# Performance work log

Measured on AMD Instinct MI355X. Metric: run time of the kernel, lower is better.

Reference implementation:

```python
import jax, jax.numpy as jnp
import numpy as np


def conv1x1(x, w, b):
    # x: [B,C,H,W], w: [O,C], b: [O] -> [B,O,H,W]
    return jnp.einsum('bchw,oc->bohw', x, w) + b[None, :, None, None]


def setup_inputs() -> dict:
    key = jax.random.key(0)
    ks = jax.random.split(key, 8)
    B, C, H, W = 16, 256, 64, 64
    Cq = C // 8
    x = jax.random.normal(ks[0], (B, C, H, W), dtype=jnp.float32)
    wq = jax.random.normal(ks[1], (Cq, C), dtype=jnp.float32) * (2.0 / C) ** 0.5
    bq = jnp.zeros((Cq,), dtype=jnp.float32)
    wk = jax.random.normal(ks[2], (Cq, C), dtype=jnp.float32) * (2.0 / C) ** 0.5
    bk = jnp.zeros((Cq,), dtype=jnp.float32)
    wv = jax.random.normal(ks[3], (C, C), dtype=jnp.float32) * (2.0 / C) ** 0.5
    bv = jnp.zeros((C,), dtype=jnp.float32)
    gamma = jax.random.normal(ks[4], (1,), dtype=jnp.float32) * 0.1
    return {'x': x, 'wq': wq, 'bq': bq, 'wk': wk, 'bk': bk, 'wv': wv, 'bv': bv, 'gamma': gamma}


def reference(x, wq, bq, wk, bk, wv, bv, gamma):
    B, C, H, W = x.shape
    bH = B // 4
    bW = B // 4  # requires bH*bW == B, i.e. B == 16
    q = conv1x1(x, wq, bq)   # [B, C/8, H, W]
    k = conv1x1(x, wk, bk)   # [B, C/8, H, W]
    v = conv1x1(x, wv, bv)   # [B, C, H, W]
    # batch index b -> grid (h = b // bW, w = b % bW); token feature = flat map
    qg = q.reshape(bH, bW, -1)  # [bH, bW, Dq]
    kg = k.reshape(bH, bW, -1)
    vg = v.reshape(bH, bW, -1)  # [bH, bW, Dv]
    # column ('H') attention with -inf diagonal, row ('W') attention
    eH = jnp.einsum('hwd,gwd->hwg', qg, kg)  # [bH, bW, bH]
    eye = jnp.eye(bH, dtype=bool)[:, None, :]  # mask h == h'
    eH = jnp.where(eye, -jnp.inf, eH)
    eW = jnp.einsum('hwd,hgd->hwg', qg, kg)  # [bH, bW, bW]
    att = jax.nn.softmax(jnp.concatenate([eH, eW], axis=-1), axis=-1)
    aH, aW = att[..., :bH], att[..., bH:]
    oH = jnp.einsum('hwg,gwd->hwd', aH, vg)  # attend down the column
    oW = jnp.einsum('hwg,hgd->hwd', aW, vg)  # attend along the row
    out = (oH + oW).reshape(B, C, H, W)
    return gamma[0] * out + x
```

## Files before the change

kernel.cpp:

```cpp
#include <hip/hip_runtime.h>

#define B_   16
#define C_   256
#define HW_  4096
#define DQK  131072
#define DV   1048576

using bf16x8  = __attribute__((ext_vector_type(8))) __bf16;
using ushort8 = __attribute__((ext_vector_type(8))) unsigned short;
using u16x4   = __attribute__((ext_vector_type(4))) unsigned short;
using f32x4   = __attribute__((ext_vector_type(4))) float;

static __device__ __forceinline__ unsigned short f2bf(float f) {
    union { float f; unsigned u; } v; v.f = f;
    unsigned r = v.u + 0x7FFFu + ((v.u >> 16) & 1u);
    return (unsigned short)(r >> 16);
}
static __device__ __forceinline__ float bf2f(unsigned short h) {
    union { unsigned u; float f; } v; v.u = ((unsigned)h) << 16;
    return v.f;
}

__global__ __launch_bounds__(256) void k_pack(const float* wq, const float* wk, const float* wv,
                                              unsigned short* Wh, unsigned short* Wl, unsigned short* Wv) {
    int idx = blockIdx.x * 256 + threadIdx.x;
    if (idx < 16384) {
        float f = (idx < 8192) ? wq[idx] : wk[idx - 8192];
        unsigned short hi = f2bf(f);
        Wh[idx] = hi;
        Wl[idx] = f2bf(f - bf2f(hi));
    } else {
        int i = idx - 16384;
        int mt = i >> 12, kt = (i >> 7) & 31, lr = (i >> 3) & 15, j = i & 7;
        int m = mt * 16 + lr, c = kt * 8 + j;
        Wv[i] = f2bf(wv[m * 256 + c]);
    }
}

__global__ __launch_bounds__(256) void k_gemm_qk(const unsigned short* __restrict__ Wh,
                                                 const unsigned short* __restrict__ Wl,
                                                 const float* __restrict__ x,
                                                 const float* __restrict__ bq, const float* __restrict__ bk,
                                                 float* __restrict__ QF, float* __restrict__ KF) {
    __shared__ __align__(16) unsigned short Ah[64][40], Al[64][40];
    __shared__ __align__(16) unsigned short Bh[128][40], Bl[128][40];
    int b  = blockIdx.y;
    int n0 = blockIdx.x * 128;
    int t = threadIdx.x;
    int lane = t & 63, wid = t >> 6;
    int wm = wid >> 1, wn = wid & 1;
    int lr = lane & 15, kg = lane >> 4;

    const float* xb = x + (size_t)b * DV;
    int am = t >> 2, akq = (t & 3) * 8;
    int bkr = t >> 3, bnq = (t & 7) * 16;
    int swz_w = (t & 3) << 3;
    int colw  = bkr ^ swz_w;

    f32x4 acc[2][4];
    for (int mi = 0; mi < 2; mi++)
        for (int ni = 0; ni < 4; ni++) acc[mi][ni] = (f32x4){0.f, 0.f, 0.f, 0.f};

    for (int kk = 0; kk < 8; kk++) {
        int k0 = kk * 32;
        *(ushort8*)&Ah[am][akq] = *(const ushort8*)(Wh + (size_t)am * 256 + k0 + akq);
        *(ushort8*)&Al[am][akq] = *(const ushort8*)(Wl + (size_t)am * 256 + k0 + akq);
        const float* srcb = xb + (size_t)(k0 + bkr) * HW_ + n0 + bnq;
        for (int e4 = 0; e4 < 4; e4++) {
            f32x4 v = *(const f32x4*)(srcb + e4 * 4);
            for (int e = 0; e < 4; e++) {
                float f = v[e];
                unsigned short hi = f2bf(f);
                int row = bnq + e4 * 4 + e;
                Bh[row][colw] = hi;
                Bl[row][colw] = f2bf(f - bf2f(hi));
            }
        }
        __syncthreads();
        bf16x8 ah[2], al[2], bh[4], bl[4];
        for (int mi = 0; mi < 2; mi++) {
            ah[mi] = *(const bf16x8*)&Ah[wm * 32 + mi * 16 + lr][kg * 8];
            al[mi] = *(const bf16x8*)&Al[wm * 32 + mi * 16 + lr][kg * 8];
        }
        for (int ni = 0; ni < 4; ni++) {
            int row = wn * 64 + ni * 16 + lr;
            int cg  = (kg ^ ((wn * 4 + ni) & 3)) * 8;
            bh[ni] = *(const bf16x8*)&Bh[row][cg];
            bl[ni] = *(const bf16x8*)&Bl[row][cg];
        }
        for (int mi = 0; mi < 2; mi++)
            for (int ni = 0; ni < 4; ni++) {
                acc[mi][ni] = __builtin_amdgcn_mfma_f32_16x16x32_bf16(ah[mi], bh[ni], acc[mi][ni], 0, 0, 0);
                acc[mi][ni] = __builtin_amdgcn_mfma_f32_16x16x32_bf16(ah[mi], bl[ni], acc[mi][ni], 0, 0, 0);
                acc[mi][ni] = __builtin_amdgcn_mfma_f32_16x16x32_bf16(al[mi], bh[ni], acc[mi][ni], 0, 0, 0);
            }
        __syncthreads();
    }
    for (int mi = 0; mi < 2; mi++) {
        int mbase = wm * 32 + mi * 16 + kg * 4;
        for (int i = 0; i < 4; i++) {
            int m = mbase + i;
            float bias = (m < 32) ? bq[m] : bk[m - 32];
            for (int ni = 0; ni < 4; ni++) {
                int n = n0 + wn * 64 + ni * 16 + lr;
                float val = acc[mi][ni][i] + bias;
                if (m < 32) QF[(size_t)b * DQK + (size_t)m * HW_ + n] = val;
                else        KF[(size_t)b * DQK + (size_t)(m - 32) * HW_ + n] = val;
            }
        }
    }
}

__global__ __launch_bounds__(256) void k_scores2(const float* __restrict__ QF, const float* __restrict__ KF,
                                                 float* __restrict__ Sp) {
    __shared__ float Ql[16][520], Kl[16][520];
    int s = blockIdx.x;
    int m = s >> 3, off = (s & 7) * 512;
    int t = threadIdx.x;
    for (int b = 0; b < 16; b++) {
        const float* qs = QF + (size_t)b * DQK + (size_t)m * HW_ + off;
        const float* ks = KF + (size_t)b * DQK + (size_t)m * HW_ + off;
        Ql[b][t]       = qs[t];
        Ql[b][t + 256] = qs[t + 256];
        Kl[b][t]       = ks[t];
        Kl[b][t + 256] = ks[t + 256];
    }
    __syncthreads();
    int p = t >> 1, h = t & 1;
    int b = p >> 3, j = p & 7;
    int hb = b >> 2, wb = b & 3;
    int bp = (j < 4) ? (j * 4 + wb) : (hb * 4 + (j - 4));
    const f32x4* q4 = (const f32x4*)&Ql[b][h * 256];
    const f32x4* k4 = (const f32x4*)&Kl[bp][h * 256];
    f32x4 a4 = (f32x4){0.f, 0.f, 0.f, 0.f};
    for (int i = 0; i < 64; i++) a4 += q4[i] * k4[i];
    float sres = a4[0] + a4[1] + a4[2] + a4[3];
    sres += __shfl_xor(sres, 1);
    if (h == 0) Sp[(size_t)p * 256 + s] = sres;
}

__global__ void k_softmax2(const float* __restrict__ Sp, const float* __restrict__ gamma,
                           float* __restrict__ Mm) {
    __shared__ float SS[128];
    int t = threadIdx.x;
    const f32x4* s4 = (const f32x4*)(Sp + (size_t)t * 256);
    f32x4 a = (f32x4){0.f, 0.f, 0.f, 0.f};
    for (int i = 0; i < 64; i++) a += s4[i];
    SS[t] = a[0] + a[1] + a[2] + a[3];
    __syncthreads();
    if (t < 16) {
        int b = t, h = b >> 2, w = b & 3;
        float e[8];
        for (int j = 0; j < 8; j++) e[j] = SS[b * 8 + j];
        e[h] = -INFINITY;
        float mx = e[0];
        for (int j = 1; j < 8; j++) mx = fmaxf(mx, e[j]);
        float aa[8], sum = 0.f;
        for (int j = 0; j < 8; j++) { aa[j] = expf(e[j] - mx); sum += aa[j]; }
        float inv = 1.0f / sum;
        float g = gamma[0];
        float row[16];
        for (int c = 0; c < 16; c++) row[c] = 0.f;
        for (int gg = 0; gg < 4; gg++) if (gg != h) row[gg * 4 + w] += aa[gg] * inv;
        for (int gg = 0; gg < 4; gg++) row[h * 4 + gg] += aa[4 + gg] * inv;
        for (int c = 0; c < 16; c++) Mm[b * 16 + c] = row[c] * g;
        Mm[256 + b] = g;
    }
}

__global__ __launch_bounds__(256) void k_mix(const float* __restrict__ Mm, const float* __restrict__ x,
                                             unsigned short* __restrict__ Xm) {
    __shared__ float Ms[256];
    __shared__ unsigned short T[16][32][36];
    int t = threadIdx.x;
    int p0 = blockIdx.x * 32, c0 = blockIdx.y * 32;
    Ms[t] = Mm[t];

    int c_l = t >> 3, p4 = t & 7;
    f32x4 in4[16];
    for (int bp = 0; bp < 16; bp++)
        in4[bp] = *(const f32x4*)(x + (size_t)bp * DV + (size_t)(c0 + c_l) * HW_ + p0 + p4 * 4);
    __syncthreads();
    for (int b = 0; b < 16; b++) {
        f32x4 acc = (f32x4){0.f, 0.f, 0.f, 0.f};
        for (int bp = 0; bp < 16; bp++) {
            float wgt = Ms[b * 16 + bp];
            acc += wgt * in4[bp];
        }
        for (int e = 0; e < 4; e++) T[b][p4 * 4 + e][c_l] = f2bf(acc[e]);
    }
    __syncthreads();
    int p_l = t >> 3, cq = t & 7;
    int p = p0 + p_l;
    int c = c0 + cq * 4;
    size_t dst = (size_t)(p >> 4) * 4096 + (size_t)(c >> 3) * 128 + (p & 15) * 8 + (c & 7);
    for (int b = 0; b < 16; b++) {
        u16x4 v = *(const u16x4*)&T[b][p_l][cq * 4];
        *(u16x4*)(Xm + (size_t)b * DV + dst) = v;
    }
}

__global__ __launch_bounds__(256) void k_gemm_v_res(const unsigned short* __restrict__ Wvf,
                                                    const unsigned short* __restrict__ Xmf,
                                                    const float* __restrict__ bv,
                                                    const float* __restrict__ MmRs,
                                                    const float* __restrict__ x,
                                                    float* __restrict__ out) {
    int b  = blockIdx.z;
    int m0 = blockIdx.y * 128;
    int n0 = blockIdx.x * 64;
    int t = threadIdx.x;
    int lane = t & 63, wid = t >> 6;
    int wm = wid >> 1, wn = wid & 1;
    int lr = lane & 15, kg = lane >> 4;

    const unsigned short* Ab = Wvf + (size_t)((m0 >> 4) + wm * 4) * 4096 + lane * 8;
    const unsigned short* Bb = Xmf + (size_t)b * DV + (size_t)((n0 >> 4) + wn * 2) * 4096 + lane * 8;

    f32x4 acc[4][2];
    for (int mi = 0; mi < 4; mi++)
        for (int ni = 0; ni < 2; ni++) acc[mi][ni] = (f32x4){0.f, 0.f, 0.f, 0.f};

    #pragma unroll 4
    for (int kk = 0; kk < 8; kk++) {
        bf16x8 a[4], bb[2];
        for (int mi = 0; mi < 4; mi++) a[mi]  = *(const bf16x8*)(Ab + (size_t)mi * 4096 + kk * 512);
        for (int ni = 0; ni < 2; ni++) bb[ni] = *(const bf16x8*)(Bb + (size_t)ni * 4096 + kk * 512);
        for (int mi = 0; mi < 4; mi++)
            for (int ni = 0; ni < 2; ni++)
                acc[mi][ni] = __builtin_amdgcn_mfma_f32_16x16x32_bf16(a[mi], bb[ni], acc[mi][ni], 0, 0, 0);
    }

    float rs_b = MmRs[256 + b];
    for (int mi = 0; mi < 4; mi++) {
        int mbase = m0 + wm * 64 + mi * 16 + kg * 4;
        for (int i = 0; i < 4; i++) {
            int m = mbase + i;
            float bias = rs_b * bv[m];
            size_t rowoff = (size_t)b * DV + (size_t)m * HW_;
            for (int ni = 0; ni < 2; ni++) {
                int n = n0 + wn * 32 + ni * 16 + lr;
                out[rowoff + n] = acc[mi][ni][i] + bias + x[rowoff + n];
            }
        }
    }
}

extern "C" void kernel_launch(void* const* d_in, const int* in_sizes, int n_in,
                              void* d_out, int out_size, void* d_ws, size_t ws_size,
                              hipStream_t stream) {
    (void)in_sizes; (void)n_in; (void)out_size; (void)ws_size;
    const float* x     = (const float*)d_in[0];
    const float* wq    = (const float*)d_in[1];
    const float* bq    = (const float*)d_in[2];
    const float* wk    = (const float*)d_in[3];
    const float* bk    = (const float*)d_in[4];
    const float* wv    = (const float*)d_in[5];
    const float* bv    = (const float*)d_in[6];
    const float* gamma = (const float*)d_in[7];

    char* ws = (char*)d_ws;
    unsigned short* Wh = (unsigned short*)(ws + 0);
    unsigned short* Wl = (unsigned short*)(ws + 32768);
    unsigned short* Wv = (unsigned short*)(ws + 65536);
    float*          QF = (float*)(ws + 196608);
    float*          KF = (float*)(ws + 8585216);
    unsigned short* Xm = (unsigned short*)(ws + 16973824);
    float*          Sp = (float*)(ws + 16973824);
    float*          Mm = (float*)(ws + 0);
    float*          vo = (float*)d_out;

    k_pack       <<<320, 256, 0, stream>>>(wq, wk, wv, Wh, Wl, Wv);
    k_gemm_qk    <<<dim3(32, 16), 256, 0, stream>>>(Wh, Wl, x, bq, bk, QF, KF);
    k_scores2    <<<256, 256, 0, stream>>>(QF, KF, Sp);
    k_softmax2   <<<1, 128, 0, stream>>>(Sp, gamma, Mm);
    k_mix        <<<dim3(128, 8), 256, 0, stream>>>(Mm, x, Xm);
    k_gemm_v_res <<<dim3(64, 2, 16), 256, 0, stream>>>(Wv, Xm, bv, Mm, x, vo);
}
```

Measured before the change: 92.39 us.

## Drop LDS staging in QK GEMM and skip zero terms in mix

The QK projection GEMM no longer stages tiles through shared memory. Weights are pre-packed into MFMA fragment order, so each lane loads its A fragments directly from global memory, and each lane gathers its B fragment from x with strided scalar loads and converts it to bf16 hi/lo in registers. The tile width is halved and the grid doubled. This removes LDS writes and both barriers, at the cost of uncoalesced strided global reads of x. Separately, the mix kernel sums only the seven row and column neighbours for each batch, skipping the mixing weights that the attention pattern makes zero.

```diff
diff --git a/kernel.cpp b/kernel.cpp
--- a/kernel.cpp
+++ b/kernel.cpp
@@ -22,90 +22,80 @@
 }
 
 __global__ __launch_bounds__(256) void k_pack(const float* wq, const float* wk, const float* wv,
-                                              unsigned short* Wh, unsigned short* Wl, unsigned short* Wv) {
+                                              unsigned short* WhF, unsigned short* WlF, unsigned short* WvF) {
     int idx = blockIdx.x * 256 + threadIdx.x;
     if (idx < 16384) {
-        float f = (idx < 8192) ? wq[idx] : wk[idx - 8192];
+        int i = idx;
+        int mt = i >> 12, cg = (i >> 7) & 31, ml = (i >> 3) & 15, cl = i & 7;
+        int m = mt * 16 + ml, c = cg * 8 + cl;
+        float f = (m < 32) ? wq[m * 256 + c] : wk[(m - 32) * 256 + c];
         unsigned short hi = f2bf(f);
-        Wh[idx] = hi;
-        Wl[idx] = f2bf(f - bf2f(hi));
+        WhF[i] = hi;
+        WlF[i] = f2bf(f - bf2f(hi));
     } else {
         int i = idx - 16384;
         int mt = i >> 12, kt = (i >> 7) & 31, lr = (i >> 3) & 15, j = i & 7;
         int m = mt * 16 + lr, c = kt * 8 + j;
-        Wv[i] = f2bf(wv[m * 256 + c]);
-    }
-}
-
-__global__ __launch_bounds__(256) void k_gemm_qk(const unsigned short* __restrict__ Wh,
-                                                 const unsigned short* __restrict__ Wl,
+        WvF[i] = f2bf(wv[m * 256 + c]);
+    }
+}
+
+__global__ __launch_bounds__(256) void k_gemm_qk(const unsigned short* __restrict__ WhF,
+                                                 const unsigned short* __restrict__ WlF,
                                                  const float* __restrict__ x,
                                                  const float* __restrict__ bq, const float* __restrict__ bk,
                                                  float* __restrict__ QF, float* __restrict__ KF) {
-    __shared__ __align__(16) unsigned short Ah[64][40], Al[64][40];
-    __shared__ __align__(16) unsigned short Bh[128][40], Bl[128][40];
     int b  = blockIdx.y;
-    int n0 = blockIdx.x * 128;
+    int n0 = blockIdx.x * 64;
     int t = threadIdx.x;
     int lane = t & 63, wid = t >> 6;
-    int wm = wid >> 1, wn = wid & 1;
+    int wm = wid & 1, wn = wid >> 1;
     int lr = lane & 15, kg = lane >> 4;
 
     const float* xb = x + (size_t)b * DV;
-    int am = t >> 2, akq = (t & 3) * 8;
-    int bkr = t >> 3, bnq = (t & 7) * 16;
-    int swz_w = (t & 3) << 3;
-    int colw  = bkr ^ swz_w;
-
-    f32x4 acc[2][4];
+    const unsigned short* Ah0 = WhF + (size_t)(wm * 2) * 4096 + lane * 8;
+    const unsigned short* Al0 = WlF + (size_t)(wm * 2) * 4096 + lane * 8;
+
+    f32x4 acc[2][2];
     for (int mi = 0; mi < 2; mi++)
-        for (int ni = 0; ni < 4; ni++) acc[mi][ni] = (f32x4){0.f, 0.f, 0.f, 0.f};
+        for (int ni = 0; ni < 2; ni++) acc[mi][ni] = (f32x4){0.f, 0.f, 0.f, 0.f};
 
     for (int kk = 0; kk < 8; kk++) {
-        int k0 = kk * 32;
-        *(ushort8*)&Ah[am][akq] = *(const ushort8*)(Wh + (size_t)am * 256 + k0 + akq);
-        *(ushort8*)&Al[am][akq] = *(const ushort8*)(Wl + (size_t)am * 256 + k0 + akq);
-        const float* srcb = xb + (size_t)(k0 + bkr) * HW_ + n0 + bnq;
-        for (int e4 = 0; e4 < 4; e4++) {
-            f32x4 v = *(const f32x4*)(srcb + e4 * 4);
-            for (int e = 0; e < 4; e++) {
-                float f = v[e];
-                unsigned short hi = f2bf(f);
-                int row = bnq + e4 * 4 + e;
-                Bh[row][colw] = hi;
-                Bl[row][colw] = f2bf(f - bf2f(hi));
-            }
-        }
-        __syncthreads();
-        bf16x8 ah[2], al[2], bh[4], bl[4];
+        bf16x8 ah[2], al[2];
         for (int mi = 0; mi < 2; mi++) {
-            ah[mi] = *(const bf16x8*)&Ah[wm * 32 + mi * 16 + lr][kg * 8];
-            al[mi] = *(const bf16x8*)&Al[wm * 32 + mi * 16 + lr][kg * 8];
-        }
-        for (int ni = 0; ni < 4; ni++) {
-            int row = wn * 64 + ni * 16 + lr;
-            int cg  = (kg ^ ((wn * 4 + ni) & 3)) * 8;
-            bh[ni] = *(const bf16x8*)&Bh[row][cg];
-            bl[ni] = *(const bf16x8*)&Bl[row][cg];
+            ah[mi] = *(const bf16x8*)(Ah0 + (size_t)mi * 4096 + kk * 512);
+            al[mi] = *(const bf16x8*)(Al0 + (size_t)mi * 4096 + kk * 512);
+        }
+        bf16x8 bh[2], bl[2];
+        int cbase = kk * 32 + kg * 8;
+        for (int ni = 0; ni < 2; ni++) {
+            const float* xp = xb + (size_t)cbase * HW_ + n0 + wn * 32 + ni * 16 + lr;
+            #pragma unroll
+            for (int j = 0; j < 8; j++) {
+                float v = xp[(size_t)j * HW_];
+                __bf16 h = (__bf16)v;
+                bh[ni][j] = h;
+                bl[ni][j] = (__bf16)(v - (float)h);
+            }
         }
         for (int mi = 0; mi < 2; mi++)
-            for (int ni = 0; ni < 4; ni++) {
+            for (int ni = 0; ni < 2; ni++) {
                 acc[mi][ni] = __builtin_amdgcn_mfma_f32_16x16x32_bf16(ah[mi], bh[ni], acc[mi][ni], 0, 0, 0);
                 acc[mi][ni] = __builtin_amdgcn_mfma_f32_16x16x32_bf16(ah[mi], bl[ni], acc[mi][ni], 0, 0, 0);
                 acc[mi][ni] = __builtin_amdgcn_mfma_f32_16x16x32_bf16(al[mi], bh[ni], acc[mi][ni], 0, 0, 0);
             }
-        __syncthreads();
-    }
+    }
+
+    float* dst = (wm == 0) ? QF : KF;
+    const float* bias = (wm == 0) ? bq : bk;
     for (int mi = 0; mi < 2; mi++) {
-        int mbase = wm * 32 + mi * 16 + kg * 4;
+        int mq0 = mi * 16 + kg * 4;
         for (int i = 0; i < 4; i++) {
-            int m = mbase + i;
-            float bias = (m < 32) ? bq[m] : bk[m - 32];
-            for (int ni = 0; ni < 4; ni++) {
-                int n = n0 + wn * 64 + ni * 16 + lr;
-                float val = acc[mi][ni][i] + bias;
-                if (m < 32) QF[(size_t)b * DQK + (size_t)m * HW_ + n] = val;
-                else        KF[(size_t)b * DQK + (size_t)(m - 32) * HW_ + n] = val;
+            int mq = mq0 + i;
+            float bs = bias[mq];
+            for (int ni = 0; ni < 2; ni++) {
+                int n = n0 + wn * 32 + ni * 16 + lr;
+                dst[(size_t)b * DQK + (size_t)mq * HW_ + n] = acc[mi][ni][i] + bs;
             }
         }
     }
@@ -182,10 +172,12 @@
         in4[bp] = *(const f32x4*)(x + (size_t)bp * DV + (size_t)(c0 + c_l) * HW_ + p0 + p4 * 4);
     __syncthreads();
     for (int b = 0; b < 16; b++) {
+        int h = b >> 2, w = b & 3;
         f32x4 acc = (f32x4){0.f, 0.f, 0.f, 0.f};
-        for (int bp = 0; bp < 16; bp++) {
-            float wgt = Ms[b * 16 + bp];
-            acc += wgt * in4[bp];
+        #pragma unroll
+        for (int g = 0; g < 4; g++) {
+            if (g != h) acc += Ms[b * 16 + g * 4 + w] * in4[g * 4 + w];
+            acc += Ms[b * 16 + h * 4 + g] * in4[h * 4 + g];
         }
         for (int e = 0; e < 4; e++) T[b][p4 * 4 + e][c_l] = f2bf(acc[e]);
     }
@@ -260,20 +252,20 @@
     const float* gamma = (const float*)d_in[7];
 
     char* ws = (char*)d_ws;
-    unsigned short* Wh = (unsigned short*)(ws + 0);
-    unsigned short* Wl = (unsigned short*)(ws + 32768);
-    unsigned short* Wv = (unsigned short*)(ws + 65536);
-    float*          QF = (float*)(ws + 196608);
-    float*          KF = (float*)(ws + 8585216);
-    unsigned short* Xm = (unsigned short*)(ws + 16973824);
-    float*          Sp = (float*)(ws + 16973824);
-    float*          Mm = (float*)(ws + 0);
-    float*          vo = (float*)d_out;
-
-    k_pack       <<<320, 256, 0, stream>>>(wq, wk, wv, Wh, Wl, Wv);
-    k_gemm_qk    <<<dim3(32, 16), 256, 0, stream>>>(Wh, Wl, x, bq, bk, QF, KF);
+    unsigned short* WhF = (unsigned short*)(ws + 0);
+    unsigned short* WlF = (unsigned short*)(ws + 32768);
+    unsigned short* WvF = (unsigned short*)(ws + 65536);
+    float*          QF  = (float*)(ws + 196608);
+    float*          KF  = (float*)(ws + 8585216);
+    unsigned short* Xm  = (unsigned short*)(ws + 16973824);
+    float*          Sp  = (float*)(ws + 16973824);
+    float*          Mm  = (float*)(ws + 0);
+    float*          vo  = (float*)d_out;
+
+    k_pack       <<<320, 256, 0, stream>>>(wq, wk, wv, WhF, WlF, WvF);
+    k_gemm_qk    <<<dim3(64, 16), 256, 0, stream>>>(WhF, WlF, x, bq, bk, QF, KF);
     k_scores2    <<<256, 256, 0, stream>>>(QF, KF, Sp);
     k_softmax2   <<<1, 128, 0, stream>>>(Sp, gamma, Mm);
     k_mix        <<<dim3(128, 8), 256, 0, stream>>>(Mm, x, Xm);
-    k_gemm_v_res <<<dim3(64, 2, 16), 256, 0, stream>>>(Wv, Xm, bv, Mm, x, vo);
-}
+    k_gemm_v_res <<<dim3(64, 2, 16), 256, 0, stream>>>(WvF, Xm, bv, Mm, x, vo);
+}
```

Result: no change. 91.11 us (-1.4%).
